# Optimization experiments

Measured on AMD Instinct MI355X. Metric: run time of the kernel, lower is better.

Reference implementation:

```python
import jax, jax.numpy as jnp
import numpy as np
import math

B, S, H, D = 2, 2048, 12, 64
DROPOUT_P = 0.1

def setup_inputs() -> dict:
    rng = jax.random.key(0)
    kq, kk, kv = jax.random.split(rng, 3)
    query = jax.random.normal(kq, (B, S, H, D), dtype=jnp.float32)
    key = jax.random.normal(kk, (B, S, H, D), dtype=jnp.float32)
    value = jax.random.normal(kv, (B, S, H, D), dtype=jnp.float32)
    return {"query": query, "key": key, "value": value}

def reference(query, key, value):
    # [B,S,H,D] -> [B,H,S,D]
    q = jnp.transpose(query, (0, 2, 1, 3))
    k = jnp.transpose(key, (0, 2, 1, 3))
    v = jnp.transpose(value, (0, 2, 1, 3))
    q = q / math.sqrt(q.shape[-1])
    # scores in fp32 (explicit cast in original)
    scores = jnp.einsum('bhsd,bhtd->bhst', q, k).astype(jnp.float32)
    attn = jax.nn.softmax(scores, axis=-1)
    # dropout (training mode in original); deterministic mask with fixed key
    keep = jax.random.bernoulli(jax.random.key(42), 1.0 - DROPOUT_P, attn.shape)
    attn = jnp.where(keep, attn / (1.0 - DROPOUT_P), 0.0)
    # explicit fp16 cast of attention weights before AV matmul
    attn = attn.astype(jnp.float16)
    out = jnp.einsum('bhst,bhtd->bhsd', attn, v)  # promotes to fp32 (v is fp32)
    return out
```

## Files before the change

kernel.cpp:

```cpp
#include <hip/hip_runtime.h>
#include <stdint.h>

#define B_ 2
#define S_ 2048
#define H_ 12
#define D_ 64
#define NKT 32
#define KEEP_THR 7549747u

typedef __attribute__((ext_vector_type(8))) _Float16 f16x8;
typedef __attribute__((ext_vector_type(4))) _Float16 f16x4;
typedef __attribute__((ext_vector_type(4))) float f32x4;

#define MFMA16 __builtin_amdgcn_mfma_f32_16x16x32_f16

__device__ __forceinline__ uint32_t rotl32(uint32_t x, uint32_t r) {
    return (x << r) | (x >> (32u - r));
}

__device__ __forceinline__ uint32_t tf_bits(uint32_t i) {
    const uint32_t k0 = 0u, k1 = 42u, k2 = 0x1BD11BF0u;
    uint32_t x0 = 0u, x1 = i;
    x0 += k0; x1 += k1;
#define TF_R(r) { x0 += x1; x1 = rotl32(x1, (r)); x1 ^= x0; }
    TF_R(13) TF_R(15) TF_R(26) TF_R(6)
    x0 += k1; x1 += k2 + 1u;
    TF_R(17) TF_R(29) TF_R(16) TF_R(24)
    x0 += k2; x1 += k0 + 2u;
    TF_R(13) TF_R(15) TF_R(26) TF_R(6)
    x0 += k0; x1 += k1 + 3u;
    TF_R(17) TF_R(29) TF_R(16) TF_R(24)
    x0 += k1; x1 += k2 + 4u;
    TF_R(13) TF_R(15) TF_R(26) TF_R(6)
    x0 += k2; x1 += k0 + 5u;
#undef TF_R
    return x0 ^ x1;
}

__global__ __launch_bounds__(256, 3)
void attn_mfma_kernel(const float* __restrict__ Q, const float* __restrict__ K,
                      const float* __restrict__ V, float* __restrict__ O) {
    __shared__ __align__(16) _Float16 Kh[64][72], Kl[64][72];
    __shared__ __align__(16) _Float16 Vh[64][72], Vl[64][72];
    __shared__ __align__(16) _Float16 PSm[4][16][72];

    const int tid  = threadIdx.x;
    const int lane = tid & 63;
    const int wid  = tid >> 6;
    const int g    = lane >> 4;
    const int sl   = lane & 15;

    const int qb = blockIdx.x & 31;
    const int bh = blockIdx.x >> 5;
    const int h  = bh % H_;
    const int b  = bh / H_;

    const int s = qb * 64 + wid * 16 + sl;
    const size_t kvbase = ((size_t)b * S_) * (H_ * D_) + (size_t)h * D_;

    f16x8 qh[2], ql[2];
    {
        const float* qp = Q + ((size_t)(b * S_ + s) * H_ + h) * D_;
#pragma unroll
        for (int ks = 0; ks < 2; ++ks) {
            int d0 = 32 * ks + 8 * g;
            float4 f0 = *reinterpret_cast<const float4*>(qp + d0);
            float4 f1 = *reinterpret_cast<const float4*>(qp + d0 + 4);
            float ff[8] = {f0.x, f0.y, f0.z, f0.w, f1.x, f1.y, f1.z, f1.w};
#pragma unroll
            for (int j = 0; j < 8; ++j) {
                float f = ff[j] * 0.125f;
                _Float16 hi = (_Float16)f;
                qh[ks][j] = hi;
                ql[ks][j] = (_Float16)(f - (float)hi);
            }
        }
    }

    const int ktK = tid >> 2;
    const int kd0 = (tid & 3) * 16;
    const int va  = tid & 7;
    const int vt0 = tid >> 3;

    float mrun = -1e30f, lrun = 0.f;
    f32x4 outacc[4];
#pragma unroll
    for (int m = 0; m < 4; ++m) outacc[m] = (f32x4){0.f, 0.f, 0.f, 0.f};

    const uint32_t flatbase = ((uint32_t)((b * H_ + h) * S_ + s)) << 11;

    for (int kt = 0; kt < NKT; ++kt) {
        if (kt) __syncthreads();
        {
            const float* kp = K + kvbase + (size_t)(kt * 64 + ktK) * (H_ * D_) + kd0;
            float4 f0 = *reinterpret_cast<const float4*>(kp);
            float4 f1 = *reinterpret_cast<const float4*>(kp + 4);
            float4 f2 = *reinterpret_cast<const float4*>(kp + 8);
            float4 f3 = *reinterpret_cast<const float4*>(kp + 12);
            float ff[16] = {f0.x, f0.y, f0.z, f0.w, f1.x, f1.y, f1.z, f1.w,
                            f2.x, f2.y, f2.z, f2.w, f3.x, f3.y, f3.z, f3.w};
            f16x8 hh0, hh1, ll0, ll1;
#pragma unroll
            for (int j = 0; j < 16; ++j) {
                _Float16 hi = (_Float16)ff[j];
                _Float16 lo = (_Float16)(ff[j] - (float)hi);
                if (j < 8) { hh0[j] = hi; ll0[j] = lo; }
                else       { hh1[j - 8] = hi; ll1[j - 8] = lo; }
            }
            *reinterpret_cast<f16x8*>(&Kh[ktK][kd0])     = hh0;
            *reinterpret_cast<f16x8*>(&Kh[ktK][kd0 + 8]) = hh1;
            *reinterpret_cast<f16x8*>(&Kl[ktK][kd0])     = ll0;
            *reinterpret_cast<f16x8*>(&Kl[ktK][kd0 + 8]) = ll1;
        }
#pragma unroll
        for (int p2 = 0; p2 < 2; ++p2) {
            int tV = vt0 + 32 * p2;
            const float* vp = V + kvbase + (size_t)(kt * 64 + tV) * (H_ * D_);
#pragma unroll
            for (int j = 0; j < 8; ++j) {
                int dd = 8 * j + va;
                float f = vp[dd];
                _Float16 hi = (_Float16)f;
                Vh[dd][tV] = hi;
                Vl[dd][tV] = (_Float16)(f - (float)hi);
            }
        }
        __syncthreads();

        f32x4 sc[4];
#pragma unroll
        for (int m = 0; m < 4; ++m) sc[m] = (f32x4){0.f, 0.f, 0.f, 0.f};
#pragma unroll
        for (int m = 0; m < 4; ++m) {
#pragma unroll
            for (int ks = 0; ks < 2; ++ks) {
                f16x8 ah = *reinterpret_cast<const f16x8*>(&Kh[16 * m + sl][8 * g + 32 * ks]);
                f16x8 al = *reinterpret_cast<const f16x8*>(&Kl[16 * m + sl][8 * g + 32 * ks]);
                sc[m] = MFMA16(ah, qh[ks], sc[m], 0, 0, 0);
                sc[m] = MFMA16(ah, ql[ks], sc[m], 0, 0, 0);
                sc[m] = MFMA16(al, qh[ks], sc[m], 0, 0, 0);
            }
        }

        float pmax = -1e30f;
#pragma unroll
        for (int m = 0; m < 4; ++m)
#pragma unroll
            for (int r = 0; r < 4; ++r) pmax = fmaxf(pmax, sc[m][r]);
        pmax = fmaxf(pmax, __shfl_xor(pmax, 16));
        pmax = fmaxf(pmax, __shfl_xor(pmax, 32));
        float mnew = fmaxf(mrun, pmax);
        float alpha = __expf(mrun - mnew);

        float p[16];
        float psum = 0.f;
#pragma unroll
        for (int m = 0; m < 4; ++m)
#pragma unroll
            for (int r = 0; r < 4; ++r) {
                float e = __expf(sc[m][r] - mnew);
                p[4 * m + r] = e;
                psum += e;
            }
        psum += __shfl_xor(psum, 16);
        psum += __shfl_xor(psum, 32);
        lrun = lrun * alpha + psum;
        mrun = mnew;
#pragma unroll
        for (int m = 0; m < 4; ++m)
#pragma unroll
            for (int r = 0; r < 4; ++r) outacc[m][r] *= alpha;

        const uint32_t fb = flatbase + (uint32_t)(kt * 64);
#pragma unroll
        for (int m = 0; m < 4; ++m) {
            int t0 = 16 * m + 4 * g;
            f16x4 w;
#pragma unroll
            for (int r = 0; r < 4; ++r) {
                uint32_t bits = tf_bits(fb + (uint32_t)(t0 + r));
                float pf = ((bits >> 9) < KEEP_THR) ? p[4 * m + r] * (1.0f / 0.9f) : 0.0f;
                w[r] = (_Float16)pf;
            }
            *reinterpret_cast<f16x4*>(&PSm[wid][sl][t0]) = w;
        }

        f16x8 pb0 = *reinterpret_cast<const f16x8*>(&PSm[wid][sl][8 * g]);
        f16x8 pb1 = *reinterpret_cast<const f16x8*>(&PSm[wid][sl][8 * g + 32]);
#pragma unroll
        for (int m = 0; m < 4; ++m) {
            f16x8 vh0 = *reinterpret_cast<const f16x8*>(&Vh[16 * m + sl][8 * g]);
            f16x8 vl0 = *reinterpret_cast<const f16x8*>(&Vl[16 * m + sl][8 * g]);
            f16x8 vh1 = *reinterpret_cast<const f16x8*>(&Vh[16 * m + sl][8 * g + 32]);
            f16x8 vl1 = *reinterpret_cast<const f16x8*>(&Vl[16 * m + sl][8 * g + 32]);
            outacc[m] = MFMA16(vh0, pb0, outacc[m], 0, 0, 0);
            outacc[m] = MFMA16(vl0, pb0, outacc[m], 0, 0, 0);
            outacc[m] = MFMA16(vh1, pb1, outacc[m], 0, 0, 0);
            outacc[m] = MFMA16(vl1, pb1, outacc[m], 0, 0, 0);
        }
    }

    const float invL = 1.0f / lrun;
    float* op = O + ((size_t)(b * H_ + h) * S_ + s) * D_;
#pragma unroll
    for (int m = 0; m < 4; ++m) {
        int dd0 = 16 * m + 4 * g;
        float4 f = make_float4(outacc[m][0] * invL, outacc[m][1] * invL,
                               outacc[m][2] * invL, outacc[m][3] * invL);
        *reinterpret_cast<float4*>(op + dd0) = f;
    }
}

extern "C" void kernel_launch(void* const* d_in, const int* in_sizes, int n_in,
                              void* d_out, int out_size, void* d_ws, size_t ws_size,
                              hipStream_t stream) {
    const float* Q = (const float*)d_in[0];
    const float* K = (const float*)d_in[1];
    const float* V = (const float*)d_in[2];
    float* O = (float*)d_out;
    (void)in_sizes; (void)n_in; (void)out_size; (void)d_ws; (void)ws_size;

    dim3 grid(B_ * H_ * (S_ / 64));
    dim3 block(256);
    attn_mfma_kernel<<<grid, block, 0, stream>>>(Q, K, V, O);
}
```

Before: 272.8 us.

## Drop K/V low-part split precision and prefetch next K/V tile into registers

Removes the fp16 hi/lo split for K and V, keeping it only for Q. This cuts the QK MFMAs from 3 to 2 and the PV MFMAs from 4 to 2 per tile, and halves the K/V shared memory. The next tile's K/V global loads are issued into registers right after the barrier so they overlap with compute, and launch bounds rise to 4 blocks per CU. The cost is lower precision in scores and output, since K and V are now rounded to fp16, which may exceed tolerance.

```diff
diff --git a/kernel.cpp b/kernel.cpp
--- a/kernel.cpp
+++ b/kernel.cpp
@@ -37,11 +37,11 @@
     return x0 ^ x1;
 }
 
-__global__ __launch_bounds__(256, 3)
+__global__ __launch_bounds__(256, 4)
 void attn_mfma_kernel(const float* __restrict__ Q, const float* __restrict__ K,
                       const float* __restrict__ V, float* __restrict__ O) {
-    __shared__ __align__(16) _Float16 Kh[64][72], Kl[64][72];
-    __shared__ __align__(16) _Float16 Vh[64][72], Vl[64][72];
+    __shared__ __align__(16) _Float16 Kh[64][72];
+    __shared__ __align__(16) _Float16 Vh[64][72];
     __shared__ __align__(16) _Float16 PSm[4][16][72];
 
     const int tid  = threadIdx.x;
@@ -80,7 +80,26 @@
     const int ktK = tid >> 2;
     const int kd0 = (tid & 3) * 16;
     const int va  = tid & 7;
-    const int vt0 = tid >> 3;
+    const int vt  = tid >> 3;
+
+    float4 ka0, ka1, ka2, ka3;
+    float vr[16];
+
+#define LOADTILE(kt_) do {                                                        \
+        const float* kp = K + kvbase + (size_t)((kt_) * 64 + ktK) * (H_ * D_) + kd0; \
+        ka0 = *reinterpret_cast<const float4*>(kp);                               \
+        ka1 = *reinterpret_cast<const float4*>(kp + 4);                           \
+        ka2 = *reinterpret_cast<const float4*>(kp + 8);                           \
+        ka3 = *reinterpret_cast<const float4*>(kp + 12);                          \
+        const float* vp = V + kvbase + (size_t)((kt_) * 64 + vt) * (H_ * D_) + va; \
+        _Pragma("unroll")                                                         \
+        for (int j = 0; j < 8; ++j) {                                             \
+            vr[j]     = vp[8 * j];                                                \
+            vr[8 + j] = vp[32 * (H_ * D_) + 8 * j];                               \
+        }                                                                         \
+    } while (0)
+
+    LOADTILE(0);
 
     float mrun = -1e30f, lrun = 0.f;
     f32x4 outacc[4];
@@ -92,40 +111,20 @@
     for (int kt = 0; kt < NKT; ++kt) {
         if (kt) __syncthreads();
         {
-            const float* kp = K + kvbase + (size_t)(kt * 64 + ktK) * (H_ * D_) + kd0;
-            float4 f0 = *reinterpret_cast<const float4*>(kp);
-            float4 f1 = *reinterpret_cast<const float4*>(kp + 4);
-            float4 f2 = *reinterpret_cast<const float4*>(kp + 8);
-            float4 f3 = *reinterpret_cast<const float4*>(kp + 12);
-            float ff[16] = {f0.x, f0.y, f0.z, f0.w, f1.x, f1.y, f1.z, f1.w,
-                            f2.x, f2.y, f2.z, f2.w, f3.x, f3.y, f3.z, f3.w};
-            f16x8 hh0, hh1, ll0, ll1;
-#pragma unroll
-            for (int j = 0; j < 16; ++j) {
-                _Float16 hi = (_Float16)ff[j];
-                _Float16 lo = (_Float16)(ff[j] - (float)hi);
-                if (j < 8) { hh0[j] = hi; ll0[j] = lo; }
-                else       { hh1[j - 8] = hi; ll1[j - 8] = lo; }
-            }
-            *reinterpret_cast<f16x8*>(&Kh[ktK][kd0])     = hh0;
-            *reinterpret_cast<f16x8*>(&Kh[ktK][kd0 + 8]) = hh1;
-            *reinterpret_cast<f16x8*>(&Kl[ktK][kd0])     = ll0;
-            *reinterpret_cast<f16x8*>(&Kl[ktK][kd0 + 8]) = ll1;
-        }
-#pragma unroll
-        for (int p2 = 0; p2 < 2; ++p2) {
-            int tV = vt0 + 32 * p2;
-            const float* vp = V + kvbase + (size_t)(kt * 64 + tV) * (H_ * D_);
-#pragma unroll
-            for (int j = 0; j < 8; ++j) {
-                int dd = 8 * j + va;
-                float f = vp[dd];
-                _Float16 hi = (_Float16)f;
-                Vh[dd][tV] = hi;
-                Vl[dd][tV] = (_Float16)(f - (float)hi);
-            }
+            float ff[16] = {ka0.x, ka0.y, ka0.z, ka0.w, ka1.x, ka1.y, ka1.z, ka1.w,
+                            ka2.x, ka2.y, ka2.z, ka2.w, ka3.x, ka3.y, ka3.z, ka3.w};
+            f16x8 h0, h1;
+#pragma unroll
+            for (int j = 0; j < 8; ++j) { h0[j] = (_Float16)ff[j]; h1[j] = (_Float16)ff[8 + j]; }
+            *reinterpret_cast<f16x8*>(&Kh[ktK][kd0])     = h0;
+            *reinterpret_cast<f16x8*>(&Kh[ktK][kd0 + 8]) = h1;
+#pragma unroll
+            for (int j = 0; j < 8; ++j) Vh[8 * j + va][vt]      = (_Float16)vr[j];
+#pragma unroll
+            for (int j = 0; j < 8; ++j) Vh[8 * j + va][vt + 32] = (_Float16)vr[8 + j];
         }
         __syncthreads();
+        if (kt + 1 < NKT) LOADTILE(kt + 1);
 
         f32x4 sc[4];
 #pragma unroll
@@ -135,10 +134,8 @@
 #pragma unroll
             for (int ks = 0; ks < 2; ++ks) {
                 f16x8 ah = *reinterpret_cast<const f16x8*>(&Kh[16 * m + sl][8 * g + 32 * ks]);
-                f16x8 al = *reinterpret_cast<const f16x8*>(&Kl[16 * m + sl][8 * g + 32 * ks]);
                 sc[m] = MFMA16(ah, qh[ks], sc[m], 0, 0, 0);
                 sc[m] = MFMA16(ah, ql[ks], sc[m], 0, 0, 0);
-                sc[m] = MFMA16(al, qh[ks], sc[m], 0, 0, 0);
             }
         }
 
@@ -151,54 +148,43 @@
         pmax = fmaxf(pmax, __shfl_xor(pmax, 32));
         float mnew = fmaxf(mrun, pmax);
         float alpha = __expf(mrun - mnew);
-
-        float p[16];
+#pragma unroll
+        for (int m = 0; m < 4; ++m)
+#pragma unroll
+            for (int r = 0; r < 4; ++r) outacc[m][r] *= alpha;
+
+        const uint32_t fb = flatbase + (uint32_t)(kt * 64);
         float psum = 0.f;
 #pragma unroll
-        for (int m = 0; m < 4; ++m)
+        for (int m = 0; m < 4; ++m) {
+            int t0 = 16 * m + 4 * g;
+            f16x4 w;
 #pragma unroll
             for (int r = 0; r < 4; ++r) {
                 float e = __expf(sc[m][r] - mnew);
-                p[4 * m + r] = e;
                 psum += e;
+                uint32_t bits = tf_bits(fb + (uint32_t)(t0 + r));
+                float pf = ((bits >> 9) < KEEP_THR) ? e * (1.0f / 0.9f) : 0.0f;
+                w[r] = (_Float16)pf;
             }
+            *reinterpret_cast<f16x4*>(&PSm[wid][sl][t0]) = w;
+        }
         psum += __shfl_xor(psum, 16);
         psum += __shfl_xor(psum, 32);
         lrun = lrun * alpha + psum;
         mrun = mnew;
-#pragma unroll
-        for (int m = 0; m < 4; ++m)
-#pragma unroll
-            for (int r = 0; r < 4; ++r) outacc[m][r] *= alpha;
-
-        const uint32_t fb = flatbase + (uint32_t)(kt * 64);
-#pragma unroll
-        for (int m = 0; m < 4; ++m) {
-            int t0 = 16 * m + 4 * g;
-            f16x4 w;
-#pragma unroll
-            for (int r = 0; r < 4; ++r) {
-                uint32_t bits = tf_bits(fb + (uint32_t)(t0 + r));
-                float pf = ((bits >> 9) < KEEP_THR) ? p[4 * m + r] * (1.0f / 0.9f) : 0.0f;
-                w[r] = (_Float16)pf;
-            }
-            *reinterpret_cast<f16x4*>(&PSm[wid][sl][t0]) = w;
-        }
 
         f16x8 pb0 = *reinterpret_cast<const f16x8*>(&PSm[wid][sl][8 * g]);
         f16x8 pb1 = *reinterpret_cast<const f16x8*>(&PSm[wid][sl][8 * g + 32]);
 #pragma unroll
         for (int m = 0; m < 4; ++m) {
             f16x8 vh0 = *reinterpret_cast<const f16x8*>(&Vh[16 * m + sl][8 * g]);
-            f16x8 vl0 = *reinterpret_cast<const f16x8*>(&Vl[16 * m + sl][8 * g]);
             f16x8 vh1 = *reinterpret_cast<const f16x8*>(&Vh[16 * m + sl][8 * g + 32]);
-            f16x8 vl1 = *reinterpret_cast<const f16x8*>(&Vl[16 * m + sl][8 * g + 32]);
             outacc[m] = MFMA16(vh0, pb0, outacc[m], 0, 0, 0);
-            outacc[m] = MFMA16(vl0, pb0, outacc[m], 0, 0, 0);
             outacc[m] = MFMA16(vh1, pb1, outacc[m], 0, 0, 0);
-            outacc[m] = MFMA16(vl1, pb1, outacc[m], 0, 0, 0);
         }
     }
+#undef LOADTILE
 
     const float invL = 1.0f / lrun;
     float* op = O + ((size_t)(b * H_ + h) * S_ + s) * D_;
```

After: 243.6 us. 1.12x faster.
